# Performance work log

Hardware: AMD Instinct MI355X
Metric: run time of the kernel (lower is better)

## Reference

```python
import jax, jax.numpy as jnp
import numpy as np

N, E, F_IN, H, C, K = 50000, 800000, 100, 128, 10, 5


def setup_inputs() -> dict:
    key = jax.random.key(0)
    ks = jax.random.split(key, 8)
    x = jax.random.normal(ks[0], (N, F_IN), jnp.float32)
    edge_index = jax.random.randint(ks[1], (2, E), 0, N, dtype=jnp.int64)
    edge_weight = jax.random.uniform(ks[2], (E,), jnp.float32)
    # Hop-wise linear weights: PyG TAGConv holds K+1 bias-free Linears per layer
    W1 = jax.random.normal(ks[3], (K + 1, F_IN, H), jnp.float32) / np.sqrt(F_IN).astype(np.float32)
    b1 = jnp.zeros((H,), jnp.float32)
    W2 = jax.random.normal(ks[4], (K + 1, H, H), jnp.float32) / np.sqrt(H).astype(np.float32)
    b2 = jnp.zeros((H,), jnp.float32)
    W3 = jax.random.normal(ks[5], (K + 1, H, C), jnp.float32) / np.sqrt(H).astype(np.float32)
    b3 = jnp.zeros((C,), jnp.float32)
    return dict(x=x, edge_index=edge_index, edge_weight=edge_weight,
                W1=W1, b1=b1, W2=W2, b2=b2, W3=W3, b3=b3)


def _gcn_norm(row, col, edge_weight, num_nodes):
    # symmetric normalization D^{-1/2} A D^{-1/2}, no self loops (TAGConv default)
    deg = jax.ops.segment_sum(edge_weight, col, num_segments=num_nodes)
    dis = jnp.where(deg > 0, jax.lax.rsqrt(jnp.maximum(deg, 1e-12)), 0.0)
    return dis[row] * edge_weight * dis[col]


def _tagconv(x, row, col, norm, W, b, num_nodes):
    # out = sum_{k=0..K} (A_norm^k x) @ W[k] + b
    out = x @ W[0] + b
    h = x
    for k in range(1, W.shape[0]):
        msg = norm[:, None] * h[row]                       # [E, d] gather
        h = jax.ops.segment_sum(msg, col, num_segments=num_nodes)  # scatter-add
        out = out + h @ W[k]
    return out


def reference(x, edge_index, edge_weight, W1, b1, W2, b2, W3, b3):
    row, col = edge_index[0], edge_index[1]
    norm = _gcn_norm(row, col, edge_weight, N)
    h = jax.nn.elu(_tagconv(x, row, col, norm, W1, b1, N))
    h = jax.nn.elu(_tagconv(h, row, col, norm, W2, b2, N))
    return _tagconv(h, row, col, norm, W3, b3, N)
```

## Files before the change

### kernel.cpp

```cpp
#include <hip/hip_runtime.h>
#include <cstdint>
#include <cstddef>

#define N_NODES 50000
#define N_EDGES 800000
#define F_IN_D 100
#define HDIM 128
#define CDIM 10
#define NCH ((N_NODES + 255) / 256)
#define NLINES 64

typedef unsigned short ushortT;

__device__ __forceinline__ float bf2f(unsigned int b16) {
  return __uint_as_float(b16 << 16);
}
__device__ __forceinline__ unsigned int f2bf(float f) {
  unsigned int u = __float_as_uint(f);
  unsigned int r = u + 0x7FFFu + ((u >> 16) & 1u);
  return r >> 16;
}

struct Args {
  const float* x; const int* ei; const float* ew;
  const float* W1; const float* b1;
  const float* W2; const float* b2;
  const float* W3; const float* b3;
  float* out;
  ushortT* Yall;
  char* A; char* B;
  ushortT* C; ushortT* D;
  int* ptrA; int* pos; int* srcs; float* wsrt;
  int* row32; int* col32; float* deg; float* dis; int* cnt; int* part;
  int* lines;
  int* gbl;
};

__device__ __forceinline__ void gbar(int* lines, int* gbl, int round, int gdim) {
  __syncthreads();
  if (threadIdx.x == 0) {
    __threadfence();
    const int perLine = gdim / NLINES;
    int old = atomicAdd(&lines[(blockIdx.x & (NLINES - 1)) * 32], 1);
    if (old == round * perLine - 1) atomicAdd(gbl, 1);
    while (__hip_atomic_load(gbl, __ATOMIC_ACQUIRE, __HIP_MEMORY_SCOPE_AGENT) < round * NLINES)
      __builtin_amdgcn_s_sleep(8);
    __threadfence();
  }
  __syncthreads();
}

template <int K_DIM, int BMODE, bool XBF, bool OUTBF>
__device__ __forceinline__ void gemm_tile(const void* __restrict__ Xv, const float* __restrict__ W,
                                          const float* __restrict__ bias, bool addb,
                                          void* __restrict__ outv, int ostride, int tile,
                                          float (&xt)[32][68], float (&bt)[32][64]) {
  const int tid = threadIdx.x;
  const int tx = tid & 15;
  const int ty = tid >> 4;
  int n0, c0;
  if (BMODE == 0) { n0 = (tile >> 1) * 64; c0 = (tile & 1) * 64; }
  else            { n0 = tile * 64;        c0 = 0; }
  float acc[4][4];
#pragma unroll
  for (int i = 0; i < 4; ++i)
#pragma unroll
    for (int j = 0; j < 4; ++j) acc[i][j] = 0.f;

  for (int k0 = 0; k0 < K_DIM; k0 += 32) {
#pragma unroll
    for (int i = 0; i < 8; ++i) {
      int idx = tid + i * 256;
      int nl = idx >> 5, kl = idx & 31;
      int nn = n0 + nl, kg = k0 + kl;
      float v = 0.f;
      if (nn < N_NODES && kg < K_DIM) {
        if (XBF) v = bf2f(((const ushortT*)Xv)[(size_t)nn * K_DIM + kg]);
        else     v = ((const float*)Xv)[(size_t)nn * K_DIM + kg];
      }
      xt[kl][nl] = v;
    }
#pragma unroll
    for (int i = 0; i < 8; ++i) {
      int idx = tid + i * 256;
      int kl = idx >> 6, cl = idx & 63;
      int kg = k0 + kl;
      float v = 0.f;
      if (BMODE == 0) {
        if (kg < K_DIM) v = W[(size_t)kg * 128 + c0 + cl];
      } else {
        if (kg < K_DIM && cl < 6 * CDIM)
          v = W[(size_t)(cl / CDIM) * (K_DIM * CDIM) + (size_t)kg * CDIM + (cl % CDIM)];
      }
      bt[kl][cl] = v;
    }
    __syncthreads();
#pragma unroll
    for (int kk = 0; kk < 32; ++kk) {
      float4 xv = *(const float4*)&xt[kk][tx * 4];
      float4 bv = *(const float4*)&bt[kk][ty * 4];
      acc[0][0] += xv.x * bv.x; acc[0][1] += xv.x * bv.y; acc[0][2] += xv.x * bv.z; acc[0][3] += xv.x * bv.w;
      acc[1][0] += xv.y * bv.x; acc[1][1] += xv.y * bv.y; acc[1][2] += xv.y * bv.z; acc[1][3] += xv.y * bv.w;
      acc[2][0] += xv.z * bv.x; acc[2][1] += xv.z * bv.y; acc[2][2] += xv.z * bv.z; acc[2][3] += xv.z * bv.w;
      acc[3][0] += xv.w * bv.x; acc[3][1] += xv.w * bv.y; acc[3][2] += xv.w * bv.z; acc[3][3] += xv.w * bv.w;
    }
    __syncthreads();
  }
#pragma unroll
  for (int i = 0; i < 4; ++i) {
    int nn = n0 + tx * 4 + i;
    if (nn >= N_NODES) continue;
#pragma unroll
    for (int j = 0; j < 4; ++j) {
      int c = c0 + ty * 4 + j;
      if (addb) {
        if (BMODE == 0) acc[i][j] += bias[c];
        else if (c < CDIM) acc[i][j] += bias[c];
      }
    }
    if (OUTBF) {
      uint2 o;
      o.x = f2bf(acc[i][0]) | (f2bf(acc[i][1]) << 16);
      o.y = f2bf(acc[i][2]) | (f2bf(acc[i][3]) << 16);
      *(uint2*)&((ushortT*)outv)[(size_t)nn * ostride + c0 + ty * 4] = o;
    } else {
#pragma unroll
      for (int j = 0; j < 4; ++j)
        ((float*)outv)[(size_t)nn * ostride + c0 + ty * 4 + j] = acc[i][j];
    }
  }
}

template <bool ELU>
__device__ __forceinline__ void hopb_phase(const uint2* __restrict__ P2, int pstr,
                                           const uint2* __restrict__ Y2, int ystr,
                                           const int* __restrict__ ptr, const int* __restrict__ srcs,
                                           const float* __restrict__ w, uint2* __restrict__ Q2) {
  const int hw = threadIdx.x >> 5;
  const int f4 = threadIdx.x & 31;
  for (int node = blockIdx.x * 8 + hw; node < N_NODES; node += gridDim.x * 8) {
    const int b = ptr[node], e = ptr[node + 1];
    uint2 yv = Y2[(size_t)node * ystr + f4];
    float a0 = bf2f(yv.x & 0xFFFFu), a1 = bf2f(yv.x >> 16);
    float a2 = bf2f(yv.y & 0xFFFFu), a3 = bf2f(yv.y >> 16);
    int j = b;
    for (; j + 15 < e; j += 16) {
      int ss[16]; float ww[16]; uint2 vv[16];
#pragma unroll
      for (int q = 0; q < 16; ++q) { ss[q] = srcs[j + q]; ww[q] = w[j + q]; }
#pragma unroll
      for (int q = 0; q < 16; ++q) vv[q] = P2[(size_t)ss[q] * pstr + f4];
#pragma unroll
      for (int q = 0; q < 16; ++q) {
        a0 += ww[q] * bf2f(vv[q].x & 0xFFFFu);
        a1 += ww[q] * bf2f(vv[q].x >> 16);
        a2 += ww[q] * bf2f(vv[q].y & 0xFFFFu);
        a3 += ww[q] * bf2f(vv[q].y >> 16);
      }
    }
    for (; j + 7 < e; j += 8) {
      int ss[8]; float ww[8]; uint2 vv[8];
#pragma unroll
      for (int q = 0; q < 8; ++q) { ss[q] = srcs[j + q]; ww[q] = w[j + q]; }
#pragma unroll
      for (int q = 0; q < 8; ++q) vv[q] = P2[(size_t)ss[q] * pstr + f4];
#pragma unroll
      for (int q = 0; q < 8; ++q) {
        a0 += ww[q] * bf2f(vv[q].x & 0xFFFFu);
        a1 += ww[q] * bf2f(vv[q].x >> 16);
        a2 += ww[q] * bf2f(vv[q].y & 0xFFFFu);
        a3 += ww[q] * bf2f(vv[q].y >> 16);
      }
    }
    for (; j + 1 < e; j += 2) {
      int s0 = srcs[j], s1 = srcs[j + 1];
      float w0 = w[j], w1 = w[j + 1];
      uint2 v0 = P2[(size_t)s0 * pstr + f4];
      uint2 v1 = P2[(size_t)s1 * pstr + f4];
      a0 += w0 * bf2f(v0.x & 0xFFFFu) + w1 * bf2f(v1.x & 0xFFFFu);
      a1 += w0 * bf2f(v0.x >> 16)     + w1 * bf2f(v1.x >> 16);
      a2 += w0 * bf2f(v0.y & 0xFFFFu) + w1 * bf2f(v1.y & 0xFFFFu);
      a3 += w0 * bf2f(v0.y >> 16)     + w1 * bf2f(v1.y >> 16);
    }
    if (j < e) {
      float w0 = w[j];
      uint2 v0 = P2[(size_t)srcs[j] * pstr + f4];
      a0 += w0 * bf2f(v0.x & 0xFFFFu);
      a1 += w0 * bf2f(v0.x >> 16);
      a2 += w0 * bf2f(v0.y & 0xFFFFu);
      a3 += w0 * bf2f(v0.y >> 16);
    }
    if (ELU) {
      a0 = a0 > 0.f ? a0 : expm1f(a0);
      a1 = a1 > 0.f ? a1 : expm1f(a1);
      a2 = a2 > 0.f ? a2 : expm1f(a2);
      a3 = a3 > 0.f ? a3 : expm1f(a3);
    }
    uint2 o;
    o.x = f2bf(a0) | (f2bf(a1) << 16);
    o.y = f2bf(a2) | (f2bf(a3) << 16);
    Q2[(size_t)node * 32 + f4] = o;
  }
}

__device__ __forceinline__ void hop10_phase(const float* __restrict__ z, int zStride, int zOff,
                                            const float* __restrict__ ybuf, int yOff,
                                            const int* __restrict__ ptr, const int* __restrict__ srcs,
                                            const float* __restrict__ wsrt, float* __restrict__ outp) {
  const int lane = threadIdx.x & 63;
  const int wid = threadIdx.x >> 6;
  const int sub = lane >> 4;
  const int f = lane & 15;
  for (int node = blockIdx.x * 4 + wid; node < N_NODES; node += gridDim.x * 4) {
    const int b = ptr[node], e = ptr[node + 1];
    const int len = e - b;
    const int js = b + (len * sub) / 4;
    const int je = b + (len * (sub + 1)) / 4;
    float acc = 0.f;
    if (f < CDIM) {
      if (sub == 0) acc = ybuf[(size_t)node * 64 + yOff + f];
      int j = js;
      for (; j + 1 < je; j += 2) {
        int s0 = srcs[j], s1 = srcs[j + 1];
        float w0 = wsrt[j], w1 = wsrt[j + 1];
        acc += w0 * z[(size_t)s0 * zStride + zOff + f] + w1 * z[(size_t)s1 * zStride + zOff + f];
      }
      if (j < je) acc += wsrt[j] * z[(size_t)srcs[j] * zStride + zOff + f];
    }
    acc += __shfl_xor(acc, 16);
    acc += __shfl_xor(acc, 32);
    if (sub == 0 && f < CDIM) outp[(size_t)node * CDIM + f] = acc;
  }
}

__global__ __launch_bounds__(256, 4) void mega_kernel(Args a) {
  __shared__ float xt[32][68];
  __shared__ float bt[32][64];
  __shared__ int sdi[256];
  const int tid = threadIdx.x;
  const int gtid = blockIdx.x * blockDim.x + tid;
  const int gstride = gridDim.x * blockDim.x;
  const int gdim = gridDim.x;
  const int TG0 = ((N_NODES + 63) / 64) * 2;
  const int TG1 = (N_NODES + 63) / 64;
  int nb = 0;

  {
    bool is64 = true;
    for (int i = 0; i < 32; ++i) if (a.ei[2 * i + 1] != 0) is64 = false;
    for (int e = gtid; e < N_EDGES; e += gstride) {
      int r, c;
      if (is64) { r = a.ei[2 * e]; c = a.ei[2 * (N_EDGES + e)]; }
      else      { r = a.ei[e];     c = a.ei[N_EDGES + e]; }
      a.row32[e] = r; a.col32[e] = c;
      atomicAdd(&a.deg[c], a.ew[e]);
      atomicAdd(&a.cnt[c], 1);
    }
  }
  for (int job = blockIdx.x; job < 6 * TG0; job += gdim) {
    int k = job / TG0, t = job % TG0;
    gemm_tile<F_IN_D, 0, false, true>(a.x, a.W1 + (size_t)k * F_IN_D * 128, a.b1, k == 0,
                                      a.Yall + k * 128, 768, t, xt, bt);
  }
  gbar(a.lines, a.gbl, ++nb, gdim);

  for (int i = gtid; i < N_NODES; i += gstride) {
    float d = a.deg[i];
    a.dis[i] = d > 0.f ? rsqrtf(fmaxf(d, 1e-12f)) : 0.f;
  }
  for (int c = blockIdx.x; c < NCH; c += gdim) {
    int i = c * 256 + tid;
    sdi[tid] = (i < N_NODES) ? a.cnt[i] : 0;
    __syncthreads();
    for (int s = 128; s > 0; s >>= 1) { if (tid < s) sdi[tid] += sdi[tid + s]; __syncthreads(); }
    if (tid == 0) a.part[c] = sdi[0];
    __syncthreads();
  }
  gbar(a.lines, a.gbl, ++nb, gdim);

  if (blockIdx.x == 0) {
    int v = (tid < NCH) ? a.part[tid] : 0;
    sdi[tid] = v;
    __syncthreads();
    for (int o = 1; o < 256; o <<= 1) {
      int t2 = (tid >= o) ? sdi[tid - o] : 0;
      __syncthreads();
      sdi[tid] += t2;
      __syncthreads();
    }
    if (tid < NCH) a.part[tid] = sdi[tid] - v;
    if (tid == 255) a.ptrA[N_NODES] = sdi[255];
  }
  gbar(a.lines, a.gbl, ++nb, gdim);

  for (int c = blockIdx.x; c < NCH; c += gdim) {
    int i = c * 256 + tid;
    int v = (i < N_NODES) ? a.cnt[i] : 0;
    sdi[tid] = v;
    __syncthreads();
    for (int o = 1; o < 256; o <<= 1) {
      int t2 = (tid >= o) ? sdi[tid - o] : 0;
      __syncthreads();
      sdi[tid] += t2;
      __syncthreads();
    }
    if (i < N_NODES) { int p = a.part[c] + sdi[tid] - v; a.ptrA[i] = p; a.pos[i] = p; }
    __syncthreads();
  }
  gbar(a.lines, a.gbl, ++nb, gdim);

  for (int e = gtid; e < N_EDGES; e += gstride) {
    int r = a.row32[e], c = a.col32[e];
    int slot = atomicAdd(&a.pos[c], 1);
    a.srcs[slot] = r;
    a.wsrt[slot] = a.dis[r] * a.ew[e] * a.dis[c];
  }
  gbar(a.lines, a.gbl, ++nb, gdim);

  const uint2* Y2 = (const uint2*)a.Yall;
  uint2* A2 = (uint2*)a.A; uint2* B2 = (uint2*)a.B;
  uint2* C2 = (uint2*)a.C; uint2* D2 = (uint2*)a.D;

  hopb_phase<false>(Y2 + 5 * 32, 192, Y2 + 4 * 32, 192, a.ptrA, a.srcs, a.wsrt, A2);
  gbar(a.lines, a.gbl, ++nb, gdim);
  hopb_phase<false>(A2, 32, Y2 + 3 * 32, 192, a.ptrA, a.srcs, a.wsrt, B2);
  gbar(a.lines, a.gbl, ++nb, gdim);
  hopb_phase<false>(B2, 32, Y2 + 2 * 32, 192, a.ptrA, a.srcs, a.wsrt, A2);
  gbar(a.lines, a.gbl, ++nb, gdim);
  hopb_phase<false>(A2, 32, Y2 + 1 * 32, 192, a.ptrA, a.srcs, a.wsrt, B2);
  gbar(a.lines, a.gbl, ++nb, gdim);
  hopb_phase<true>(B2, 32, Y2 + 0 * 32, 192, a.ptrA, a.srcs, a.wsrt, C2);
  gbar(a.lines, a.gbl, ++nb, gdim);

  for (int job = blockIdx.x; job < 6 * TG0; job += gdim) {
    int k = job / TG0, t = job % TG0;
    gemm_tile<HDIM, 0, true, true>(a.C, a.W2 + (size_t)k * HDIM * 128, a.b2, k == 0,
                                   a.Yall + k * 128, 768, t, xt, bt);
  }
  gbar(a.lines, a.gbl, ++nb, gdim);
  hopb_phase<false>(Y2 + 5 * 32, 192, Y2 + 4 * 32, 192, a.ptrA, a.srcs, a.wsrt, A2);
  gbar(a.lines, a.gbl, ++nb, gdim);
  hopb_phase<false>(A2, 32, Y2 + 3 * 32, 192, a.ptrA, a.srcs, a.wsrt, B2);
  gbar(a.lines, a.gbl, ++nb, gdim);
  hopb_phase<false>(B2, 32, Y2 + 2 * 32, 192, a.ptrA, a.srcs, a.wsrt, A2);
  gbar(a.lines, a.gbl, ++nb, gdim);
  hopb_phase<false>(A2, 32, Y2 + 1 * 32, 192, a.ptrA, a.srcs, a.wsrt, B2);
  gbar(a.lines, a.gbl, ++nb, gdim);
  hopb_phase<true>(B2, 32, Y2 + 0 * 32, 192, a.ptrA, a.srcs, a.wsrt, D2);
  gbar(a.lines, a.gbl, ++nb, gdim);

  float* ybuf = (float*)a.A;
  float* z0 = (float*)a.B;
  float* z1 = (float*)(a.B + (size_t)N_NODES * 16 * 4);
  for (int t = blockIdx.x; t < TG1; t += gdim)
    gemm_tile<HDIM, 1, true, false>(a.D, a.W3, a.b3, true, ybuf, 64, t, xt, bt);
  gbar(a.lines, a.gbl, ++nb, gdim);
  hop10_phase(ybuf, 64, 50, ybuf, 40, a.ptrA, a.srcs, a.wsrt, z0); gbar(a.lines, a.gbl, ++nb, gdim);
  hop10_phase(z0, 10, 0, ybuf, 30, a.ptrA, a.srcs, a.wsrt, z1); gbar(a.lines, a.gbl, ++nb, gdim);
  hop10_phase(z1, 10, 0, ybuf, 20, a.ptrA, a.srcs, a.wsrt, z0); gbar(a.lines, a.gbl, ++nb, gdim);
  hop10_phase(z0, 10, 0, ybuf, 10, a.ptrA, a.srcs, a.wsrt, z1); gbar(a.lines, a.gbl, ++nb, gdim);
  hop10_phase(z1, 10, 0, ybuf, 0, a.ptrA, a.srcs, a.wsrt, a.out);
}


extern "C" void kernel_launch(void* const* d_in, const int* in_sizes, int n_in,
                              void* d_out, int out_size, void* d_ws, size_t ws_size,
                              hipStream_t stream) {
  Args a;
  a.x  = (const float*)d_in[0];
  a.ei = (const int*)d_in[1];
  a.ew = (const float*)d_in[2];
  a.W1 = (const float*)d_in[3];
  a.b1 = (const float*)d_in[4];
  a.W2 = (const float*)d_in[5];
  a.b2 = (const float*)d_in[6];
  a.W3 = (const float*)d_in[7];
  a.b3 = (const float*)d_in[8];
  a.out = (float*)d_out;

  const int N = N_NODES, E = N_EDGES;
  char* base = (char*)d_ws;
  size_t off = 0;
  auto alloc = [&](size_t bytes) -> char* {
    char* p = base + off;
    off += (bytes + 255) & ~(size_t)255;
    return p;
  };
  a.Yall = (ushortT*)alloc((size_t)N * 768 * 2);
  a.A = alloc((size_t)N * 256);
  a.B = alloc((size_t)N * 256);
  a.C = (ushortT*)alloc((size_t)N * 128 * 2);
  a.D = (ushortT*)alloc((size_t)N * 128 * 2);
  a.ptrA = (int*)alloc((size_t)(N + 1) * 4);
  a.pos  = (int*)alloc((size_t)N * 4);
  a.srcs = (int*)alloc((size_t)E * 4);
  a.wsrt = (float*)alloc((size_t)E * 4);
  a.lines = (int*)alloc(NLINES * 32 * 4);
  a.gbl   = (int*)alloc(256);

  char* t = a.A;
  a.row32 = (int*)t;            t += (size_t)E * 4;
  a.col32 = (int*)t;            t += (size_t)E * 4;
  a.deg   = (float*)t;          t += (size_t)N * 4;
  a.dis   = (float*)t;          t += (size_t)N * 4;
  a.cnt   = (int*)t;            t += (size_t)N * 4;
  a.part  = (int*)t;            t += 2048 * 4;

  hipMemsetAsync(a.lines, 0, NLINES * 32 * 4, stream);
  hipMemsetAsync(a.gbl, 0, 256, stream);
  hipMemsetAsync(a.deg, 0, (size_t)N * 4, stream);
  hipMemsetAsync(a.cnt, 0, (size_t)N * 4, stream);

  int occ = 0;
  hipOccupancyMaxActiveBlocksPerMultiprocessor(&occ, (const void*)mega_kernel, 256, 0);
  if (occ < 1) occ = 1;
  int grid = occ * 256;
  if (grid > 2048) grid = 2048;
  if (grid < 64) grid = 64;
  grid &= ~(NLINES - 1);

  void* args[] = { &a };
  hipLaunchCooperativeKernel((const void*)mega_kernel, dim3(grid), dim3(256), args, 0, stream);

  (void)in_sizes; (void)n_in; (void)out_size; (void)ws_size;
}
```

Measured before the change: 4.268 ms.

## Partition edge CSR by source slab to improve gather locality in hop phases

Builds a second CSR keyed by (source slab, destination), with 8 source slabs. Each block now owns a contiguous node range and processes it slab by slab, keeping per-node accumulators in shared memory, so gathers at any moment hit a smaller source window that fits better in cache. The extra counting, scanning and scatter passes add preprocessing cost, and the grid cap drops to 1024 blocks. Shared memory grows to 52x128 floats per block, which may reduce occupancy, and the static block partition may load-balance worse than the old strided loop.

```diff
diff --git a/kernel.cpp b/kernel.cpp
--- a/kernel.cpp
+++ b/kernel.cpp
@@ -7,8 +7,13 @@
 #define F_IN_D 100
 #define HDIM 128
 #define CDIM 10
+#define NSLAB 8
+#define SLABN (N_NODES / NSLAB)
+#define NKEY (NSLAB * N_NODES)
 #define NCH ((N_NODES + 255) / 256)
+#define NCH2 ((NKEY + 255) / 256)
 #define NLINES 64
+#define NBC 52
 
 typedef unsigned short ushortT;
 
@@ -31,9 +36,10 @@
   char* A; char* B;
   ushortT* C; ushortT* D;
   int* ptrA; int* pos; int* srcs; float* wsrt;
+  int* ptr2; int* pos2; int* srcs2; float* wsrt2;
   int* row32; int* col32; float* deg; float* dis; int* cnt; int* part;
-  int* lines;
-  int* gbl;
+  int* cnt2; int* part2;
+  int* lines; int* gbl;
 };
 
 __device__ __forceinline__ void gbar(int* lines, int* gbl, int round, int gdim) {
@@ -54,7 +60,7 @@
 __device__ __forceinline__ void gemm_tile(const void* __restrict__ Xv, const float* __restrict__ W,
                                           const float* __restrict__ bias, bool addb,
                                           void* __restrict__ outv, int ostride, int tile,
-                                          float (&xt)[32][68], float (&bt)[32][64]) {
+                                          float (*xt)[68], float (*bt)[64]) {
   const int tid = threadIdx.x;
   const int tx = tid & 15;
   const int ty = tid >> 4;
@@ -132,74 +138,76 @@
 }
 
 template <bool ELU>
-__device__ __forceinline__ void hopb_phase(const uint2* __restrict__ P2, int pstr,
-                                           const uint2* __restrict__ Y2, int ystr,
-                                           const int* __restrict__ ptr, const int* __restrict__ srcs,
-                                           const float* __restrict__ w, uint2* __restrict__ Q2) {
+__device__ __forceinline__ void hops5_phase(const uint2* __restrict__ P2, int pstr, int pOff,
+                                            const uint2* __restrict__ Y2, int ystr, int yOff,
+                                            const int* __restrict__ ptr2, const int* __restrict__ srcs2,
+                                            const float* __restrict__ w2, uint2* __restrict__ Q2,
+                                            float (*acc)[128], int n0, int n1) {
   const int hw = threadIdx.x >> 5;
   const int f4 = threadIdx.x & 31;
-  for (int node = blockIdx.x * 8 + hw; node < N_NODES; node += gridDim.x * 8) {
-    const int b = ptr[node], e = ptr[node + 1];
-    uint2 yv = Y2[(size_t)node * ystr + f4];
-    float a0 = bf2f(yv.x & 0xFFFFu), a1 = bf2f(yv.x >> 16);
-    float a2 = bf2f(yv.y & 0xFFFFu), a3 = bf2f(yv.y >> 16);
-    int j = b;
-    for (; j + 15 < e; j += 16) {
-      int ss[16]; float ww[16]; uint2 vv[16];
-#pragma unroll
-      for (int q = 0; q < 16; ++q) { ss[q] = srcs[j + q]; ww[q] = w[j + q]; }
-#pragma unroll
-      for (int q = 0; q < 16; ++q) vv[q] = P2[(size_t)ss[q] * pstr + f4];
-#pragma unroll
-      for (int q = 0; q < 16; ++q) {
-        a0 += ww[q] * bf2f(vv[q].x & 0xFFFFu);
-        a1 += ww[q] * bf2f(vv[q].x >> 16);
-        a2 += ww[q] * bf2f(vv[q].y & 0xFFFFu);
-        a3 += ww[q] * bf2f(vv[q].y >> 16);
-      }
-    }
-    for (; j + 7 < e; j += 8) {
-      int ss[8]; float ww[8]; uint2 vv[8];
-#pragma unroll
-      for (int q = 0; q < 8; ++q) { ss[q] = srcs[j + q]; ww[q] = w[j + q]; }
-#pragma unroll
-      for (int q = 0; q < 8; ++q) vv[q] = P2[(size_t)ss[q] * pstr + f4];
-#pragma unroll
-      for (int q = 0; q < 8; ++q) {
-        a0 += ww[q] * bf2f(vv[q].x & 0xFFFFu);
-        a1 += ww[q] * bf2f(vv[q].x >> 16);
-        a2 += ww[q] * bf2f(vv[q].y & 0xFFFFu);
-        a3 += ww[q] * bf2f(vv[q].y >> 16);
-      }
-    }
-    for (; j + 1 < e; j += 2) {
-      int s0 = srcs[j], s1 = srcs[j + 1];
-      float w0 = w[j], w1 = w[j + 1];
-      uint2 v0 = P2[(size_t)s0 * pstr + f4];
-      uint2 v1 = P2[(size_t)s1 * pstr + f4];
-      a0 += w0 * bf2f(v0.x & 0xFFFFu) + w1 * bf2f(v1.x & 0xFFFFu);
-      a1 += w0 * bf2f(v0.x >> 16)     + w1 * bf2f(v1.x >> 16);
-      a2 += w0 * bf2f(v0.y & 0xFFFFu) + w1 * bf2f(v1.y & 0xFFFFu);
-      a3 += w0 * bf2f(v0.y >> 16)     + w1 * bf2f(v1.y >> 16);
-    }
-    if (j < e) {
-      float w0 = w[j];
-      uint2 v0 = P2[(size_t)srcs[j] * pstr + f4];
-      a0 += w0 * bf2f(v0.x & 0xFFFFu);
-      a1 += w0 * bf2f(v0.x >> 16);
-      a2 += w0 * bf2f(v0.y & 0xFFFFu);
-      a3 += w0 * bf2f(v0.y >> 16);
-    }
-    if (ELU) {
-      a0 = a0 > 0.f ? a0 : expm1f(a0);
-      a1 = a1 > 0.f ? a1 : expm1f(a1);
-      a2 = a2 > 0.f ? a2 : expm1f(a2);
-      a3 = a3 > 0.f ? a3 : expm1f(a3);
-    }
-    uint2 o;
-    o.x = f2bf(a0) | (f2bf(a1) << 16);
-    o.y = f2bf(a2) | (f2bf(a3) << 16);
-    Q2[(size_t)node * 32 + f4] = o;
+  const int fb = f4 * 4;
+  for (int c0n = n0; c0n < n1; c0n += NBC) {
+    const int c1n = (c0n + NBC < n1) ? c0n + NBC : n1;
+    for (int n = c0n + hw; n < c1n; n += 8) {
+      uint2 yv = Y2[(size_t)n * ystr + yOff + f4];
+      int li = n - c0n;
+      acc[li][fb + 0] = bf2f(yv.x & 0xFFFFu);
+      acc[li][fb + 1] = bf2f(yv.x >> 16);
+      acc[li][fb + 2] = bf2f(yv.y & 0xFFFFu);
+      acc[li][fb + 3] = bf2f(yv.y >> 16);
+    }
+    for (int p = 0; p < NSLAB; ++p) {
+      const int keyBase = p * N_NODES;
+      for (int n = c0n + hw; n < c1n; n += 8) {
+        const int b = ptr2[keyBase + n], e = ptr2[keyBase + n + 1];
+        if (b == e) continue;
+        const int li = n - c0n;
+        float a0 = acc[li][fb + 0], a1 = acc[li][fb + 1];
+        float a2 = acc[li][fb + 2], a3 = acc[li][fb + 3];
+        int j = b;
+        for (; j + 3 < e; j += 4) {
+          int s0 = srcs2[j], s1 = srcs2[j + 1], s2 = srcs2[j + 2], s3 = srcs2[j + 3];
+          float w0 = w2[j], w1 = w2[j + 1], w2v = w2[j + 2], w3 = w2[j + 3];
+          uint2 v0 = P2[(size_t)s0 * pstr + pOff + f4];
+          uint2 v1 = P2[(size_t)s1 * pstr + pOff + f4];
+          uint2 v2 = P2[(size_t)s2 * pstr + pOff + f4];
+          uint2 v3 = P2[(size_t)s3 * pstr + pOff + f4];
+          a0 += w0 * bf2f(v0.x & 0xFFFFu) + w1 * bf2f(v1.x & 0xFFFFu)
+              + w2v * bf2f(v2.x & 0xFFFFu) + w3 * bf2f(v3.x & 0xFFFFu);
+          a1 += w0 * bf2f(v0.x >> 16) + w1 * bf2f(v1.x >> 16)
+              + w2v * bf2f(v2.x >> 16) + w3 * bf2f(v3.x >> 16);
+          a2 += w0 * bf2f(v0.y & 0xFFFFu) + w1 * bf2f(v1.y & 0xFFFFu)
+              + w2v * bf2f(v2.y & 0xFFFFu) + w3 * bf2f(v3.y & 0xFFFFu);
+          a3 += w0 * bf2f(v0.y >> 16) + w1 * bf2f(v1.y >> 16)
+              + w2v * bf2f(v2.y >> 16) + w3 * bf2f(v3.y >> 16);
+        }
+        for (; j < e; ++j) {
+          float w0 = w2[j];
+          uint2 v0 = P2[(size_t)srcs2[j] * pstr + pOff + f4];
+          a0 += w0 * bf2f(v0.x & 0xFFFFu);
+          a1 += w0 * bf2f(v0.x >> 16);
+          a2 += w0 * bf2f(v0.y & 0xFFFFu);
+          a3 += w0 * bf2f(v0.y >> 16);
+        }
+        acc[li][fb + 0] = a0; acc[li][fb + 1] = a1;
+        acc[li][fb + 2] = a2; acc[li][fb + 3] = a3;
+      }
+    }
+    for (int n = c0n + hw; n < c1n; n += 8) {
+      int li = n - c0n;
+      float a0 = acc[li][fb + 0], a1 = acc[li][fb + 1];
+      float a2 = acc[li][fb + 2], a3 = acc[li][fb + 3];
+      if (ELU) {
+        a0 = a0 > 0.f ? a0 : expm1f(a0);
+        a1 = a1 > 0.f ? a1 : expm1f(a1);
+        a2 = a2 > 0.f ? a2 : expm1f(a2);
+        a3 = a3 > 0.f ? a3 : expm1f(a3);
+      }
+      uint2 o;
+      o.x = f2bf(a0) | (f2bf(a1) << 16);
+      o.y = f2bf(a2) | (f2bf(a3) << 16);
+      Q2[(size_t)n * 32 + f4] = o;
+    }
   }
 }
 
@@ -233,16 +241,42 @@
   }
 }
 
+__device__ __forceinline__ void scan_partials(int* partial, int nb, int* tot, int totIdx, int* sdi) {
+  const int tid = threadIdx.x;
+  int carry = 0;
+  for (int base = 0; base < nb; base += 256) {
+    int i = base + tid;
+    int v = (i < nb) ? partial[i] : 0;
+    sdi[tid] = v;
+    __syncthreads();
+    for (int o = 1; o < 256; o <<= 1) {
+      int t2 = (tid >= o) ? sdi[tid - o] : 0;
+      __syncthreads();
+      sdi[tid] += t2;
+      __syncthreads();
+    }
+    if (i < nb) partial[i] = carry + sdi[tid] - v;
+    carry += sdi[255];
+    __syncthreads();
+  }
+  if (tid == 0) tot[totIdx] = carry;
+}
+
 __global__ __launch_bounds__(256, 4) void mega_kernel(Args a) {
-  __shared__ float xt[32][68];
-  __shared__ float bt[32][64];
-  __shared__ int sdi[256];
+  __shared__ float smemf[NBC * 128];
+  float (*xt)[68] = (float(*)[68])smemf;
+  float (*bt)[64] = (float(*)[64])(smemf + 32 * 68);
+  int* sdi = (int*)smemf;
+  float (*accL)[128] = (float(*)[128])smemf;
   const int tid = threadIdx.x;
   const int gtid = blockIdx.x * blockDim.x + tid;
   const int gstride = gridDim.x * blockDim.x;
   const int gdim = gridDim.x;
   const int TG0 = ((N_NODES + 63) / 64) * 2;
   const int TG1 = (N_NODES + 63) / 64;
+  const int NB = (N_NODES + gdim - 1) / gdim;
+  const int n0 = blockIdx.x * NB;
+  const int n1 = (n0 + NB < N_NODES) ? n0 + NB : N_NODES;
   int nb = 0;
 
   {
@@ -255,6 +289,7 @@
       a.row32[e] = r; a.col32[e] = c;
       atomicAdd(&a.deg[c], a.ew[e]);
       atomicAdd(&a.cnt[c], 1);
+      atomicAdd(&a.cnt2[(r / SLABN) * N_NODES + c], 1);
     }
   }
   for (int job = blockIdx.x; job < 6 * TG0; job += gdim) {
@@ -276,21 +311,18 @@
     if (tid == 0) a.part[c] = sdi[0];
     __syncthreads();
   }
-  gbar(a.lines, a.gbl, ++nb, gdim);
-
-  if (blockIdx.x == 0) {
-    int v = (tid < NCH) ? a.part[tid] : 0;
-    sdi[tid] = v;
-    __syncthreads();
-    for (int o = 1; o < 256; o <<= 1) {
-      int t2 = (tid >= o) ? sdi[tid - o] : 0;
-      __syncthreads();
-      sdi[tid] += t2;
-      __syncthreads();
-    }
-    if (tid < NCH) a.part[tid] = sdi[tid] - v;
-    if (tid == 255) a.ptrA[N_NODES] = sdi[255];
-  }
+  for (int c = blockIdx.x; c < NCH2; c += gdim) {
+    int i = c * 256 + tid;
+    sdi[tid] = (i < NKEY) ? a.cnt2[i] : 0;
+    __syncthreads();
+    for (int s = 128; s > 0; s >>= 1) { if (tid < s) sdi[tid] += sdi[tid + s]; __syncthreads(); }
+    if (tid == 0) a.part2[c] = sdi[0];
+    __syncthreads();
+  }
+  gbar(a.lines, a.gbl, ++nb, gdim);
+
+  if (blockIdx.x == 0) scan_partials(a.part, NCH, a.ptrA, N_NODES, sdi);
+  if (blockIdx.x == 1) scan_partials(a.part2, NCH2, a.ptr2, NKEY, sdi);
   gbar(a.lines, a.gbl, ++nb, gdim);
 
   for (int c = blockIdx.x; c < NCH; c += gdim) {
@@ -307,13 +339,32 @@
     if (i < N_NODES) { int p = a.part[c] + sdi[tid] - v; a.ptrA[i] = p; a.pos[i] = p; }
     __syncthreads();
   }
+  for (int c = blockIdx.x; c < NCH2; c += gdim) {
+    int i = c * 256 + tid;
+    int v = (i < NKEY) ? a.cnt2[i] : 0;
+    sdi[tid] = v;
+    __syncthreads();
+    for (int o = 1; o < 256; o <<= 1) {
+      int t2 = (tid >= o) ? sdi[tid - o] : 0;
+      __syncthreads();
+      sdi[tid] += t2;
+      __syncthreads();
+    }
+    if (i < NKEY) { int p = a.part2[c] + sdi[tid] - v; a.ptr2[i] = p; a.pos2[i] = p; }
+    __syncthreads();
+  }
   gbar(a.lines, a.gbl, ++nb, gdim);
 
   for (int e = gtid; e < N_EDGES; e += gstride) {
     int r = a.row32[e], c = a.col32[e];
+    float nrm = a.dis[r] * a.ew[e] * a.dis[c];
     int slot = atomicAdd(&a.pos[c], 1);
     a.srcs[slot] = r;
-    a.wsrt[slot] = a.dis[r] * a.ew[e] * a.dis[c];
+    a.wsrt[slot] = nrm;
+    int key = (r / SLABN) * N_NODES + c;
+    int slot2 = atomicAdd(&a.pos2[key], 1);
+    a.srcs2[slot2] = r;
+    a.wsrt2[slot2] = nrm;
   }
   gbar(a.lines, a.gbl, ++nb, gdim);
 
@@ -321,15 +372,15 @@
   uint2* A2 = (uint2*)a.A; uint2* B2 = (uint2*)a.B;
   uint2* C2 = (uint2*)a.C; uint2* D2 = (uint2*)a.D;
 
-  hopb_phase<false>(Y2 + 5 * 32, 192, Y2 + 4 * 32, 192, a.ptrA, a.srcs, a.wsrt, A2);
-  gbar(a.lines, a.gbl, ++nb, gdim);
-  hopb_phase<false>(A2, 32, Y2 + 3 * 32, 192, a.ptrA, a.srcs, a.wsrt, B2);
-  gbar(a.lines, a.gbl, ++nb, gdim);
-  hopb_phase<false>(B2, 32, Y2 + 2 * 32, 192, a.ptrA, a.srcs, a.wsrt, A2);
-  gbar(a.lines, a.gbl, ++nb, gdim);
-  hopb_phase<false>(A2, 32, Y2 + 1 * 32, 192, a.ptrA, a.srcs, a.wsrt, B2);
-  gbar(a.lines, a.gbl, ++nb, gdim);
-  hopb_phase<true>(B2, 32, Y2 + 0 * 32, 192, a.ptrA, a.srcs, a.wsrt, C2);
+  hops5_phase<false>(Y2, 192, 5 * 32, Y2, 192, 4 * 32, a.ptr2, a.srcs2, a.wsrt2, A2, accL, n0, n1);
+  gbar(a.lines, a.gbl, ++nb, gdim);
+  hops5_phase<false>(A2, 32, 0, Y2, 192, 3 * 32, a.ptr2, a.srcs2, a.wsrt2, B2, accL, n0, n1);
+  gbar(a.lines, a.gbl, ++nb, gdim);
+  hops5_phase<false>(B2, 32, 0, Y2, 192, 2 * 32, a.ptr2, a.srcs2, a.wsrt2, A2, accL, n0, n1);
+  gbar(a.lines, a.gbl, ++nb, gdim);
+  hops5_phase<false>(A2, 32, 0, Y2, 192, 1 * 32, a.ptr2, a.srcs2, a.wsrt2, B2, accL, n0, n1);
+  gbar(a.lines, a.gbl, ++nb, gdim);
+  hops5_phase<true>(B2, 32, 0, Y2, 192, 0, a.ptr2, a.srcs2, a.wsrt2, C2, accL, n0, n1);
   gbar(a.lines, a.gbl, ++nb, gdim);
 
   for (int job = blockIdx.x; job < 6 * TG0; job += gdim) {
@@ -338,15 +389,15 @@
                                    a.Yall + k * 128, 768, t, xt, bt);
   }
   gbar(a.lines, a.gbl, ++nb, gdim);
-  hopb_phase<false>(Y2 + 5 * 32, 192, Y2 + 4 * 32, 192, a.ptrA, a.srcs, a.wsrt, A2);
-  gbar(a.lines, a.gbl, ++nb, gdim);
-  hopb_phase<false>(A2, 32, Y2 + 3 * 32, 192, a.ptrA, a.srcs, a.wsrt, B2);
-  gbar(a.lines, a.gbl, ++nb, gdim);
-  hopb_phase<false>(B2, 32, Y2 + 2 * 32, 192, a.ptrA, a.srcs, a.wsrt, A2);
-  gbar(a.lines, a.gbl, ++nb, gdim);
-  hopb_phase<false>(A2, 32, Y2 + 1 * 32, 192, a.ptrA, a.srcs, a.wsrt, B2);
-  gbar(a.lines, a.gbl, ++nb, gdim);
-  hopb_phase<true>(B2, 32, Y2 + 0 * 32, 192, a.ptrA, a.srcs, a.wsrt, D2);
+  hops5_phase<false>(Y2, 192, 5 * 32, Y2, 192, 4 * 32, a.ptr2, a.srcs2, a.wsrt2, A2, accL, n0, n1);
+  gbar(a.lines, a.gbl, ++nb, gdim);
+  hops5_phase<false>(A2, 32, 0, Y2, 192, 3 * 32, a.ptr2, a.srcs2, a.wsrt2, B2, accL, n0, n1);
+  gbar(a.lines, a.gbl, ++nb, gdim);
+  hops5_phase<false>(B2, 32, 0, Y2, 192, 2 * 32, a.ptr2, a.srcs2, a.wsrt2, A2, accL, n0, n1);
+  gbar(a.lines, a.gbl, ++nb, gdim);
+  hops5_phase<false>(A2, 32, 0, Y2, 192, 1 * 32, a.ptr2, a.srcs2, a.wsrt2, B2, accL, n0, n1);
+  gbar(a.lines, a.gbl, ++nb, gdim);
+  hops5_phase<true>(B2, 32, 0, Y2, 192, 0, a.ptr2, a.srcs2, a.wsrt2, D2, accL, n0, n1);
   gbar(a.lines, a.gbl, ++nb, gdim);
 
   float* ybuf = (float*)a.A;
@@ -395,6 +446,10 @@
   a.pos  = (int*)alloc((size_t)N * 4);
   a.srcs = (int*)alloc((size_t)E * 4);
   a.wsrt = (float*)alloc((size_t)E * 4);
+  a.ptr2 = (int*)alloc((size_t)(NKEY + 1) * 4);
+  a.pos2 = (int*)alloc((size_t)NKEY * 4);
+  a.srcs2 = (int*)alloc((size_t)E * 4);
+  a.wsrt2 = (float*)alloc((size_t)E * 4);
   a.lines = (int*)alloc(NLINES * 32 * 4);
   a.gbl   = (int*)alloc(256);
 
@@ -405,19 +460,23 @@
   a.dis   = (float*)t;          t += (size_t)N * 4;
   a.cnt   = (int*)t;            t += (size_t)N * 4;
   a.part  = (int*)t;            t += 2048 * 4;
+  char* t2 = a.B;
+  a.cnt2  = (int*)t2;           t2 += (size_t)NKEY * 4;
+  a.part2 = (int*)t2;           t2 += 2048 * 4;
 
   hipMemsetAsync(a.lines, 0, NLINES * 32 * 4, stream);
   hipMemsetAsync(a.gbl, 0, 256, stream);
   hipMemsetAsync(a.deg, 0, (size_t)N * 4, stream);
   hipMemsetAsync(a.cnt, 0, (size_t)N * 4, stream);
+  hipMemsetAsync(a.cnt2, 0, (size_t)NKEY * 4, stream);
 
   int occ = 0;
   hipOccupancyMaxActiveBlocksPerMultiprocessor(&occ, (const void*)mega_kernel, 256, 0);
   if (occ < 1) occ = 1;
   int grid = occ * 256;
-  if (grid > 2048) grid = 2048;
-  if (grid < 64) grid = 64;
+  if (grid > 1024) grid = 1024;
   grid &= ~(NLINES - 1);
+  if (grid < NLINES) grid = NLINES;
 
   void* args[] = { &a };
   hipLaunchCooperativeKernel((const void*)mega_kernel, dim3(grid), dim3(256), args, 0, stream);
```

Result: slower. 5.925 ms (+38.8%).
